# Kernel tuning notes

Hardware: AMD Instinct MI355X
Metric: run time of the kernel (lower is better)

## Reference

```python
import jax, jax.numpy as jnp
import numpy as np

EPS = 1e-5

def _bn(t, gamma, beta):
    # training-mode BatchNorm2d: stats over (B,H,W), biased variance
    mean = jnp.mean(t, axis=(0, 2, 3), keepdims=True)
    var = jnp.var(t, axis=(0, 2, 3), keepdims=True)
    tn = (t - mean) * jax.lax.rsqrt(var + EPS)
    return tn * gamma[None, :, None, None] + beta[None, :, None, None]

def setup_inputs() -> dict:
    key = jax.random.key(0)
    ks = jax.random.split(key, 8)
    B, C, H, W = 16, 256, 64, 64
    u, k, v = 4, 16, 256
    s = 1.0 / np.sqrt(C)
    x = jax.random.normal(ks[0], (B, C, H, W), dtype=jnp.float32)
    Wq = jax.random.normal(ks[1], (k, C), dtype=jnp.float32) * s
    bq = jax.random.normal(ks[2], (k,), dtype=jnp.float32) * 0.01
    Wk = jax.random.normal(ks[3], (u * k, C), dtype=jnp.float32) * s
    bk = jax.random.normal(ks[4], (u * k,), dtype=jnp.float32) * 0.01
    Wv = jax.random.normal(ks[5], (u * v, C), dtype=jnp.float32) * s
    bv = jax.random.normal(ks[6], (u * v,), dtype=jnp.float32) * 0.01
    gamma_q = jnp.ones((k,), dtype=jnp.float32)
    beta_q = jnp.zeros((k,), dtype=jnp.float32)
    gamma_v = jnp.ones((u * v,), dtype=jnp.float32)
    beta_v = jnp.zeros((u * v,), dtype=jnp.float32)
    return {"x": x, "Wq": Wq, "bq": bq, "Wk": Wk, "bk": bk, "Wv": Wv, "bv": bv,
            "gamma_q": gamma_q, "beta_q": beta_q, "gamma_v": gamma_v, "beta_v": beta_v}

def reference(x, Wq, bq, Wk, bk, Wv, bv, gamma_q, beta_q, gamma_v, beta_v):
    B, C, H, W = x.shape
    k = Wq.shape[0]
    u = 4
    v = Wv.shape[0] // u
    # 1x1 convs as channel contractions
    Q = jnp.einsum('oc,bchw->bohw', Wq, x) + bq[None, :, None, None]   # [B,k,H,W]
    K = jnp.einsum('oc,bchw->bohw', Wk, x) + bk[None, :, None, None]   # [B,u*k,H,W]
    V = jnp.einsum('oc,bchw->bohw', Wv, x) + bv[None, :, None, None]   # [B,u*v,H,W]
    Q = _bn(Q, gamma_q, beta_q)
    V = _bn(V, gamma_v, beta_v)
    m = H * W
    Q = Q.reshape(B, k, m)          # [B,k,m]
    K = K.reshape(B, u, k, m)       # [B,u,k,m]
    V = V.reshape(B, u, v, m)       # [B,u,v,m]
    K = jax.nn.softmax(K, axis=3)
    context = jnp.einsum('bukm,buvm->bkv', K, V)   # [B,k,v]
    y = jnp.einsum('bkn,bkv->bvn', Q, context)     # [B,v,m]
    return y.reshape(B, v, H, W)
```

## Files before the change

### kernel.cpp

```cpp
#include <hip/hip_runtime.h>
#include <hip/hip_bf16.h>

typedef short s16x8 __attribute__((ext_vector_type(8)));
typedef short s16x4 __attribute__((ext_vector_type(4)));
typedef float f32x4 __attribute__((ext_vector_type(4)));
typedef unsigned u32;
typedef u32 u32x2 __attribute__((ext_vector_type(2)));

#define DI __device__ __forceinline__

constexpr int BB = 16;
constexpr int CC = 256;
constexpr int MM = 4096;
constexpr int KD = 16;
constexpr int UK = 64;
constexpr float EPSV = 1e-5f;

DI unsigned short f2bf(float f) {
  union { float f; unsigned u; } v; v.f = f;
  unsigned r = v.u + 0x7FFFu + ((v.u >> 16) & 1u);
  return (unsigned short)(r >> 16);
}
DI float bfu(unsigned short u) { union { u32 u; float f; } w; w.u = (u32)u << 16; return w.f; }
DI float bflo(u32 v) { union { u32 u; float f; } w; w.u = v << 16; return w.f; }
DI float bfhi(u32 v) { union { u32 u; float f; } w; w.u = v & 0xFFFF0000u; return w.f; }

__global__ __launch_bounds__(256) void k_cvt(const float* __restrict__ x,
    unsigned short* __restrict__ xbf, float* __restrict__ xsump) {
  int bid = blockIdx.x;
  size_t base = (size_t)bid * MM;
  int t = threadIdx.x;
  float s = 0.f;
#pragma unroll
  for (int i = 0; i < 4; ++i) {
    size_t idx = base + (size_t)(i * 256 + t) * 4;
    float4 v = *(const float4*)(x + idx);
    s16x4 c;
    c[0] = (short)f2bf(v.x); c[1] = (short)f2bf(v.y);
    c[2] = (short)f2bf(v.z); c[3] = (short)f2bf(v.w);
    *(s16x4*)&xbf[idx] = c;
    s += v.x + v.y + v.z + v.w;
  }
#pragma unroll
  for (int o = 32; o; o >>= 1) s += __shfl_down(s, o);
  __shared__ float red[4];
  if ((t & 63) == 0) red[t >> 6] = s;
  __syncthreads();
  if (t == 0) xsump[bid] = red[0] + red[1] + red[2] + red[3];
}

__global__ __launch_bounds__(512) void k_gxx(const unsigned short* __restrict__ xbf,
                                             u32* __restrict__ part) {
  int b = blockIdx.x >> 4, mc = blockIdx.x & 15;
  int m0 = mc * 256;
  __shared__ short lds[2][256 * 72];
  int t = threadIdx.x, w = t >> 6, l = t & 63;
  int wr = w >> 2, wc = w & 3;
  int lrow = l & 15, lk8 = (l >> 4) * 8;
  int srow = t >> 3, sseg = (t & 7) * 8;

  const unsigned short* gsrc = xbf + ((size_t)(b * CC + srow)) * MM + m0 + sseg;

  s16x8 rg[4];
#pragma unroll
  for (int i = 0; i < 4; ++i)
    rg[i] = *(const s16x8*)(gsrc + (size_t)i * 64 * MM);
#pragma unroll
  for (int i = 0; i < 4; ++i)
    *(s16x8*)&lds[0][(srow + i * 64) * 72 + sseg] = rg[i];

  f32x4 acc[8][4];
#pragma unroll
  for (int i = 0; i < 8; ++i)
#pragma unroll
    for (int j = 0; j < 4; ++j) acc[i][j] = (f32x4)0.f;

#pragma unroll
  for (int ks = 0; ks < 4; ++ks) {
    __syncthreads();
    if (ks < 3) {
#pragma unroll
      for (int i = 0; i < 4; ++i)
        rg[i] = *(const s16x8*)(gsrc + (size_t)i * 64 * MM + (ks + 1) * 64);
    }
    int buf = ks & 1;
#pragma unroll
    for (int half = 0; half < 2; ++half) {
      s16x8 af[8], bf[4];
#pragma unroll
      for (int i = 0; i < 8; ++i)
        af[i] = *(const s16x8*)&lds[buf][(wr * 128 + i * 16 + lrow) * 72 + half * 32 + lk8];
#pragma unroll
      for (int j = 0; j < 4; ++j)
        bf[j] = *(const s16x8*)&lds[buf][(wc * 64 + j * 16 + lrow) * 72 + half * 32 + lk8];
#pragma unroll
      for (int i = 0; i < 8; ++i)
#pragma unroll
        for (int j = 0; j < 4; ++j)
          acc[i][j] = __builtin_amdgcn_mfma_f32_16x16x32_bf16(af[i], bf[j], acc[i][j], 0, 0, 0);
    }
    if (ks < 3) {
#pragma unroll
      for (int i = 0; i < 4; ++i)
        *(s16x8*)&lds[buf ^ 1][(srow + i * 64) * 72 + sseg] = rg[i];
    }
  }

  size_t pb = (size_t)blockIdx.x * 32768;
#pragma unroll
  for (int i = 0; i < 8; ++i)
#pragma unroll
    for (int j = 0; j < 4; ++j) {
      int tau = (w * 8 + i) * 4 + j;
      u32x2 pk;
      pk[0] = (u32)f2bf(acc[i][j][0]) | ((u32)f2bf(acc[i][j][1]) << 16);
      pk[1] = (u32)f2bf(acc[i][j][2]) | ((u32)f2bf(acc[i][j][3]) << 16);
      *(u32x2*)&part[pb + tau * 128 + l * 2] = pk;
    }
}

__global__ __launch_bounds__(256) void k_gred(const u32* __restrict__ part,
                                              float* __restrict__ G) {
  int q = blockIdx.x * 256 + threadIdx.x;
  float s0 = 0.f, s1 = 0.f;
#pragma unroll 8
  for (int p = 0; p < 256; ++p) {
    u32 v = part[(size_t)p * 32768 + q];
    s0 += bflo(v);
    s1 += bfhi(v);
  }
  int r2 = q & 1, l = (q >> 1) & 63, tau = q >> 7;
  int j = tau & 3, i = (tau >> 2) & 7, w = tau >> 5;
  int wr = w >> 2, wc = w & 3;
  int row = wr * 128 + i * 16 + (l >> 4) * 4 + r2 * 2;
  int col = wc * 64 + j * 16 + (l & 15);
  G[row * 256 + col] = s0;
  G[(row + 1) * 256 + col] = s1;
}

__global__ __launch_bounds__(256) void k_proj(const unsigned short* __restrict__ xbf,
    const float* __restrict__ Wq, const float* __restrict__ bq,
    const float* __restrict__ Wk, const float* __restrict__ bk,
    unsigned short* __restrict__ Kbf, unsigned short* __restrict__ Qbf,
    float* __restrict__ pstat) {
  int b = blockIdx.x >> 5, mc = blockIdx.x & 31;
  int gm0 = mc * 128;
  __shared__ short wlds[80 * 264];
  __shared__ u32 xt[128 * 17];
  __shared__ float smax[4][64], ssum[4][64];
  int t = threadIdx.x;
  int w = t >> 6, l = t & 63;
  int lrow = l & 15, lk = l >> 4;

#pragma unroll 4
  for (int o = 0; o < 80; ++o) {
    float v = (o < 64) ? Wk[o * CC + t] : Wq[(o - 64) * CC + t];
    wlds[o * 264 + t] = (short)f2bf(v);
  }

  f32x4 acc[5][2];
#pragma unroll
  for (int i = 0; i < 5; ++i) { acc[i][0] = (f32x4)0.f; acc[i][1] = (f32x4)0.f; }

  int c2 = t >> 4;
  int mq = t & 15;

  for (int ks = 0; ks < 8; ++ks) {
    int c0 = ks * 32;
    __syncthreads();
#pragma unroll
    for (int mb = 0; mb < 128; mb += 64) {
      int m = mb + mq * 4;
      const unsigned short* p0 = xbf + ((size_t)(b * CC + c0 + 2 * c2)) * MM + gm0 + m;
      s16x4 v0 = *(const s16x4*)p0;
      s16x4 v1 = *(const s16x4*)(p0 + MM);
      xt[(m + 0) * 17 + c2] = (u32)(unsigned short)v0[0] | ((u32)(unsigned short)v1[0] << 16);
      xt[(m + 1) * 17 + c2] = (u32)(unsigned short)v0[1] | ((u32)(unsigned short)v1[1] << 16);
      xt[(m + 2) * 17 + c2] = (u32)(unsigned short)v0[2] | ((u32)(unsigned short)v1[2] << 16);
      xt[(m + 3) * 17 + c2] = (u32)(unsigned short)v0[3] | ((u32)(unsigned short)v1[3] << 16);
    }
    __syncthreads();
    union { s16x8 v; u32 wd[4]; } bfr[2];
#pragma unroll
    for (int j = 0; j < 2; ++j) {
      int ml = w * 32 + j * 16 + lrow;
#pragma unroll
      for (int i = 0; i < 4; ++i) bfr[j].wd[i] = xt[ml * 17 + lk * 4 + i];
    }
#pragma unroll
    for (int ot = 0; ot < 5; ++ot) {
      s16x8 af = *(const s16x8*)&wlds[(ot * 16 + lrow) * 264 + c0 + lk * 8];
      acc[ot][0] = __builtin_amdgcn_mfma_f32_16x16x32_bf16(af, bfr[0].v, acc[ot][0], 0, 0, 0);
      acc[ot][1] = __builtin_amdgcn_mfma_f32_16x16x32_bf16(af, bfr[1].v, acc[ot][1], 0, 0, 0);
    }
  }

  int mcol = gm0 + w * 32 + lrow;
#pragma unroll
  for (int ot = 0; ot < 4; ++ot)
#pragma unroll
    for (int r = 0; r < 4; ++r) {
      int o = ot * 16 + lk * 4 + r;
      float bias = bk[o];
      unsigned short u0 = f2bf(acc[ot][0][r] + bias);
      unsigned short u1 = f2bf(acc[ot][1][r] + bias);
      size_t rowoff = ((size_t)(b * UK + o)) * MM;
      Kbf[rowoff + mcol] = u0;
      Kbf[rowoff + mcol + 16] = u1;
      float rv0 = bfu(u0), rv1 = bfu(u1);
      float mx = fmaxf(rv0, rv1);
      mx = fmaxf(mx, __shfl_xor(mx, 1));
      mx = fmaxf(mx, __shfl_xor(mx, 2));
      mx = fmaxf(mx, __shfl_xor(mx, 4));
      mx = fmaxf(mx, __shfl_xor(mx, 8));
      float se = __expf(rv0 - mx) + __expf(rv1 - mx);
      se += __shfl_xor(se, 1);
      se += __shfl_xor(se, 2);
      se += __shfl_xor(se, 4);
      se += __shfl_xor(se, 8);
      if (lrow == 0) { smax[w][o] = mx; ssum[w][o] = se; }
    }
#pragma unroll
  for (int r = 0; r < 4; ++r) {
    int oq = lk * 4 + r;
    float bias = bq[oq];
    size_t rowoff = ((size_t)(b * KD + oq)) * MM;
    Qbf[rowoff + mcol] = f2bf(acc[4][0][r] + bias);
    Qbf[rowoff + mcol + 16] = f2bf(acc[4][1][r] + bias);
  }
  __syncthreads();
  if (t < 64) {
    float m0_ = smax[0][t], m1_ = smax[1][t], m2_ = smax[2][t], m3_ = smax[3][t];
    float mm = fmaxf(fmaxf(m0_, m1_), fmaxf(m2_, m3_));
    float ss = ssum[0][t] * __expf(m0_ - mm) + ssum[1][t] * __expf(m1_ - mm) +
               ssum[2][t] * __expf(m2_ - mm) + ssum[3][t] * __expf(m3_ - mm);
    size_t po = ((size_t)blockIdx.x * 64 + t) * 2;
    pstat[po] = mm;
    pstat[po + 1] = ss;
  }
}

__global__ __launch_bounds__(64) void k_pmerge(const float* __restrict__ pstat,
    float* __restrict__ rmax, float* __restrict__ rsum) {
  int b = blockIdx.x, o = threadIdx.x;
  float mm = -3.4e38f;
#pragma unroll 8
  for (int mc = 0; mc < 32; ++mc)
    mm = fmaxf(mm, pstat[((size_t)((b * 32 + mc) * 64 + o)) * 2]);
  float ss = 0.f;
#pragma unroll 8
  for (int mc = 0; mc < 32; ++mc) {
    size_t po = ((size_t)((b * 32 + mc) * 64 + o)) * 2;
    ss += pstat[po + 1] * __expf(pstat[po] - mm);
  }
  rmax[b * 64 + o] = mm;
  rsum[b * 64 + o] = ss;
}

__global__ __launch_bounds__(256) void k_fin(const float* __restrict__ G,
    const float* __restrict__ xsump,
    const float* __restrict__ Wv, const float* __restrict__ bv,
    const float* __restrict__ gv, const float* __restrict__ btv,
    const float* __restrict__ Wq, const float* __restrict__ bq,
    const float* __restrict__ gq, const float* __restrict__ btq,
    float* __restrict__ AV, float* __restrict__ BVa,
    float* __restrict__ AQ, float* __restrict__ BQa) {
  int t = threadIdx.x, w = t >> 6, l = t & 63;
  int o0 = blockIdx.x * 4;
  __shared__ float lw[4][256];
#pragma unroll
  for (int oo = 0; oo < 4; ++oo) {
    int o = o0 + oo;
    lw[oo][t] = (o < 1024) ? Wv[(size_t)o * CC + t] : Wq[(size_t)(o - 1024) * CC + t];
  }
  __syncthreads();

  float4 w4[4];
#pragma unroll
  for (int oo = 0; oo < 4; ++oo) w4[oo] = *(const float4*)&lw[oo][4 * l];

  float qf[4] = {0.f, 0.f, 0.f, 0.f};
#pragma unroll 4
  for (int i = 0; i < 64; ++i) {
    int r = i * 4 + w;
    float4 g4 = *(const float4*)(G + (size_t)r * CC + 4 * l);
#pragma unroll
    for (int oo = 0; oo < 4; ++oo) {
      float d = g4.x * w4[oo].x + g4.y * w4[oo].y + g4.z * w4[oo].z + g4.w * w4[oo].w;
      qf[oo] = fmaf(lw[oo][r], d, qf[oo]);
    }
  }

  float xs = 0.f;
#pragma unroll
  for (int bb = 0; bb < 16; ++bb) xs += xsump[bb * 256 + t];
  float sx[4];
#pragma unroll
  for (int oo = 0; oo < 4; ++oo) sx[oo] = lw[oo][t] * xs;

#pragma unroll
  for (int oo = 0; oo < 4; ++oo)
#pragma unroll
    for (int od = 32; od; od >>= 1) {
      qf[oo] += __shfl_xor(qf[oo], od);
      sx[oo] += __shfl_xor(sx[oo], od);
    }
  __shared__ float rq[4][4], rs[4][4];
  if (l == 0)
#pragma unroll
    for (int oo = 0; oo < 4; ++oo) { rq[w][oo] = qf[oo]; rs[w][oo] = sx[oo]; }
  __syncthreads();
  if (t < 4) {
    int oo = t, o = o0 + oo;
    float q = rq[0][oo] + rq[1][oo] + rq[2][oo] + rq[3][oo];
    float s = rs[0][oo] + rs[1][oo] + rs[2][oo] + rs[3][oo];
    float bias, gamma, beta; float *pa, *pb;
    if (o < 1024) { bias = bv[o]; gamma = gv[o]; beta = btv[o]; pa = AV + o; pb = BVa + o; }
    else { int oi = o - 1024; bias = bq[oi]; gamma = gq[oi]; beta = btq[oi]; pa = AQ + oi; pb = BQa + oi; }
    const float invN = 1.f / 65536.f;
    float mean = s * invN + bias;
    float e2 = q * invN + 2.f * bias * s * invN + bias * bias;
    float var = e2 - mean * mean;
    float a = gamma * rsqrtf(var + EPSV);
    *pa = a;
    *pb = beta - mean * a;
  }
}

__global__ __launch_bounds__(256) void k_xp(const unsigned short* __restrict__ xbf,
    const unsigned short* __restrict__ Kbf, const float* __restrict__ rmax,
    float* __restrict__ xpp) {
  int b = blockIdx.x >> 4, kc = blockIdx.x & 15;
  int kbase = kc * 256;
  __shared__ short la[64][40];
  __shared__ short lb[256][40];
  int t = threadIdx.x, w = t >> 6, l = t & 63;
  int lrow = l & 15, lk = (l >> 4) * 8;

  f32x4 acc[4][4];
#pragma unroll
  for (int i = 0; i < 4; ++i)
#pragma unroll
    for (int j = 0; j < 4; ++j) acc[i][j] = (f32x4)0.f;

  for (int ks = 0; ks < 8; ++ks) {
    int k0 = kbase + ks * 32;
    __syncthreads();
    {
      int r = t >> 2, sg = (t & 3) * 8;
      s16x8 kv = *(const s16x8*)&Kbf[((size_t)(b * UK + r)) * MM + k0 + sg];
      float rm = rmax[b * UK + r];
      s16x8 wv;
#pragma unroll
      for (int i = 0; i < 8; ++i)
        wv[i] = (short)f2bf(__expf(bfu((unsigned short)kv[i]) - rm));
      *(s16x8*)&la[r][sg] = wv;
    }
#pragma unroll
    for (int i = 0; i < 4; ++i) {
      int r = i * 64 + (t >> 2), sg = (t & 3) * 8;
      s16x8 v = *(const s16x8*)&xbf[((size_t)(b * CC + r)) * MM + k0 + sg];
      *(s16x8*)&lb[r][sg] = v;
    }
    __syncthreads();
    s16x8 af[4], bfr[4];
#pragma unroll
    for (int i = 0; i < 4; ++i) af[i] = *(const s16x8*)&la[i * 16 + lrow][lk];
#pragma unroll
    for (int j = 0; j < 4; ++j) bfr[j] = *(const s16x8*)&lb[w * 64 + j * 16 + lrow][lk];
#pragma unroll
    for (int i = 0; i < 4; ++i)
#pragma unroll
      for (int j = 0; j < 4; ++j)
        acc[i][j] = __builtin_amdgcn_mfma_f32_16x16x32_bf16(af[i], bfr[j], acc[i][j], 0, 0, 0);
  }
  float* dst = xpp + (size_t)blockIdx.x * UK * CC;
#pragma unroll
  for (int i = 0; i < 4; ++i)
#pragma unroll
    for (int j = 0; j < 4; ++j)
#pragma unroll
      for (int r = 0; r < 4; ++r) {
        int row = i * 16 + (l >> 4) * 4 + r;
        int col = w * 64 + j * 16 + lrow;
        dst[row * 256 + col] = acc[i][j][r];
      }
}

__global__ __launch_bounds__(256) void k_prep(const float* __restrict__ xpp,
    const float* __restrict__ rsum, const float* __restrict__ Wv,
    const float* __restrict__ AV, unsigned short* __restrict__ xpn,
    unsigned short* __restrict__ wvs) {
  int t = threadIdx.x;
  if (blockIdx.x < 256) {
    int b = blockIdx.x >> 4, kk = blockIdx.x & 15;
    unsigned short* dst = xpn + ((size_t)(b * 16 + kk)) * 1024;
#pragma unroll
    for (int u = 0; u < 4; ++u) {
      int row = u * 16 + kk;
      float s = 0.f;
#pragma unroll
      for (int kc = 0; kc < 16; ++kc)
        s += xpp[((size_t)(b * 16 + kc) * UK + row) * CC + t];
      s /= rsum[b * UK + row];
      dst[u * 256 + t] = f2bf(s);
    }
  } else {
    int ch = blockIdx.x - 256;
    float a = AV[ch];
    wvs[(size_t)ch * CC + t] = f2bf(a * Wv[(size_t)ch * CC + t]);
  }
}

__global__ __launch_bounds__(64) void k_ctx2(const unsigned short* __restrict__ xpn,
    const unsigned short* __restrict__ wvs,
    const float* __restrict__ AV, const float* __restrict__ bv,
    const float* __restrict__ BVa, float* __restrict__ CTX) {
  int mt = blockIdx.x >> 3, nt = blockIdx.x & 7;
  int m0 = mt * 32, n0 = nt * 32;
  int l = threadIdx.x;
  int lrow = l & 15, lk8 = (l >> 4) * 8;

  f32x4 acc[2][2];
#pragma unroll
  for (int i = 0; i < 2; ++i)
#pragma unroll
    for (int j = 0; j < 2; ++j) acc[i][j] = (f32x4)0.f;

#pragma unroll 4
  for (int k0 = 0; k0 < 1024; k0 += 32) {
    int u = k0 >> 8, c0 = k0 & 255;
    s16x8 a0 = *(const s16x8*)&xpn[(size_t)(m0 + lrow) * 1024 + k0 + lk8];
    s16x8 a1 = *(const s16x8*)&xpn[(size_t)(m0 + 16 + lrow) * 1024 + k0 + lk8];
    s16x8 b0 = *(const s16x8*)&wvs[(size_t)(u * 256 + n0 + lrow) * CC + c0 + lk8];
    s16x8 b1 = *(const s16x8*)&wvs[(size_t)(u * 256 + n0 + 16 + lrow) * CC + c0 + lk8];
    acc[0][0] = __builtin_amdgcn_mfma_f32_16x16x32_bf16(a0, b0, acc[0][0], 0, 0, 0);
    acc[0][1] = __builtin_amdgcn_mfma_f32_16x16x32_bf16(a0, b1, acc[0][1], 0, 0, 0);
    acc[1][0] = __builtin_amdgcn_mfma_f32_16x16x32_bf16(a1, b0, acc[1][0], 0, 0, 0);
    acc[1][1] = __builtin_amdgcn_mfma_f32_16x16x32_bf16(a1, b1, acc[1][1], 0, 0, 0);
  }

  float cst[2];
#pragma unroll
  for (int j = 0; j < 2; ++j) {
    int vv = n0 + j * 16 + lrow;
    float s = 0.f;
#pragma unroll
    for (int u = 0; u < 4; ++u) {
      int ch = u * 256 + vv;
      s += AV[ch] * bv[ch] + BVa[ch];
    }
    cst[j] = s;
  }

#pragma unroll
  for (int i = 0; i < 2; ++i)
#pragma unroll
    for (int j = 0; j < 2; ++j)
#pragma unroll
      for (int r = 0; r < 4; ++r) {
        int row = m0 + i * 16 + (l >> 4) * 4 + r;
        int col = n0 + j * 16 + lrow;
        CTX[(size_t)row * 256 + col] = acc[i][j][r] + cst[j];
      }
}

__global__ __launch_bounds__(256) void k_y(const unsigned short* __restrict__ Qbf,
    const float* __restrict__ CTX,
    const float* __restrict__ AQ, const float* __restrict__ BQa,
    float* __restrict__ y) {
  int b = blockIdx.x >> 4, nc = blockIdx.x & 15;
  int m = nc * 256 + threadIdx.x;
  float qn[16];
#pragma unroll
  for (int kk = 0; kk < 16; ++kk)
    qn[kk] = AQ[kk] * bfu(Qbf[((size_t)b * KD + kk) * MM + m]) + BQa[kk];
  const float* cb = CTX + (size_t)b * KD * 256;
  float* yo = y + (size_t)b * 256 * MM + m;
#pragma unroll 4
  for (int vv = 0; vv < 256; ++vv) {
    float acc = 0.f;
#pragma unroll
    for (int kk = 0; kk < 16; ++kk)
      acc = fmaf(qn[kk], cb[kk * 256 + vv], acc);
    yo[(size_t)vv * MM] = acc;
  }
}

extern "C" void kernel_launch(void* const* d_in, const int* in_sizes, int n_in,
                              void* d_out, int out_size, void* d_ws, size_t ws_size,
                              hipStream_t stream) {
  const float* x   = (const float*)d_in[0];
  const float* Wq  = (const float*)d_in[1];
  const float* bq  = (const float*)d_in[2];
  const float* Wk  = (const float*)d_in[3];
  const float* bk  = (const float*)d_in[4];
  const float* Wv  = (const float*)d_in[5];
  const float* bv  = (const float*)d_in[6];
  const float* gq  = (const float*)d_in[7];
  const float* btq = (const float*)d_in[8];
  const float* gv  = (const float*)d_in[9];
  const float* btv = (const float*)d_in[10];
  float* out = (float*)d_out;
  float* ws  = (float*)d_ws;

  float* G     = ws;
  float* XSUMP = ws + 65536;
  float* PSTAT = ws + 69632;
  float* RMAX  = ws + 135168;
  float* RSUM  = ws + 136192;
  float* AV    = ws + 137216;
  float* BVa   = ws + 138240;
  float* AQ    = ws + 139264;
  float* BQa   = ws + 139280;
  float* CTX   = ws + 139520;
  u32*  PART   = (u32*)(ws + 205056);
  float* XPP   = ws + 205056;
  unsigned short* KBf = (unsigned short*)(ws + 4399360);
  unsigned short* QBf = (unsigned short*)(ws + 6496512);
  unsigned short* XBF = (unsigned short*)(ws + 8593664);
  unsigned short* XPN = (unsigned short*)(ws + 16982272);
  unsigned short* WVS = (unsigned short*)(ws + 17113344);

  k_cvt   <<<4096, 256, 0, stream>>>(x, XBF, XSUMP);
  k_gxx   <<<256,  512, 0, stream>>>(XBF, PART);
  k_gred  <<<128,  256, 0, stream>>>(PART, G);
  k_proj  <<<512,  256, 0, stream>>>(XBF, Wq, bq, Wk, bk, KBf, QBf, PSTAT);
  k_pmerge<<<16,   64,  0, stream>>>(PSTAT, RMAX, RSUM);
  k_fin   <<<260,  256, 0, stream>>>(G, XSUMP, Wv, bv, gv, btv, Wq, bq, gq, btq,
                                     AV, BVa, AQ, BQa);
  k_xp    <<<256,  256, 0, stream>>>(XBF, KBf, RMAX, XPP);
  k_prep  <<<1280, 256, 0, stream>>>(XPP, RSUM, Wv, AV, XPN, WVS);
  k_ctx2  <<<64,   64,  0, stream>>>(XPN, WVS, AV, bv, BVa, CTX);
  k_y     <<<256,  256, 0, stream>>>(QBf, CTX, AQ, BQa, out);
}
```

Before: 151.2 us.

## Double-buffer x and weight tiles in k_proj with register prefetch

The projection kernel used to stage all 80x256 weights into LDS before the main loop, then load each x tile with two barriers per k-step. It now streams weight slices per k-step alongside x, using two LDS buffers and register prefetch of the next step's global loads while MFMAs run on the current buffer. This cuts the up-front weight staging, shrinks LDS use and halves the barriers per step. In exchange it uses more registers and converts each weight slice to bf16 again in every block.

```diff
diff --git a/kernel.cpp b/kernel.cpp
--- a/kernel.cpp
+++ b/kernel.cpp
@@ -145,54 +145,111 @@
     float* __restrict__ pstat) {
   int b = blockIdx.x >> 5, mc = blockIdx.x & 31;
   int gm0 = mc * 128;
-  __shared__ short wlds[80 * 264];
-  __shared__ u32 xt[128 * 17];
+  __shared__ u32 xt[2][128 * 17];
+  __shared__ short wb[2][80 * 40];
   __shared__ float smax[4][64], ssum[4][64];
   int t = threadIdx.x;
   int w = t >> 6, l = t & 63;
   int lrow = l & 15, lk = l >> 4;
-
-#pragma unroll 4
-  for (int o = 0; o < 80; ++o) {
-    float v = (o < 64) ? Wk[o * CC + t] : Wq[(o - 64) * CC + t];
-    wlds[o * 264 + t] = (short)f2bf(v);
-  }
-
-  f32x4 acc[5][2];
-#pragma unroll
-  for (int i = 0; i < 5; ++i) { acc[i][0] = (f32x4)0.f; acc[i][1] = (f32x4)0.f; }
-
   int c2 = t >> 4;
   int mq = t & 15;
+  int wrow0 = t >> 3;
+  int wcol = (t & 7) * 4;
+
+  s16x4 xv[2][2];
+  float4 wv[3];
+
+  {
+    const unsigned short* p0 = xbf + ((size_t)(b * CC + 2 * c2)) * MM + gm0 + mq * 4;
+#pragma unroll
+    for (int mb = 0; mb < 2; ++mb) {
+      xv[mb][0] = *(const s16x4*)(p0 + mb * 64);
+      xv[mb][1] = *(const s16x4*)(p0 + mb * 64 + MM);
+    }
+#pragma unroll
+    for (int rep = 0; rep < 3; ++rep) {
+      int row = rep * 32 + wrow0;
+      if (row < 80)
+        wv[rep] = *(const float4*)((row < 64 ? Wk + (size_t)row * CC
+                                             : Wq + (size_t)(row - 64) * CC) + wcol);
+    }
+#pragma unroll
+    for (int mb = 0; mb < 2; ++mb) {
+      int m = mb * 64 + mq * 4;
+#pragma unroll
+      for (int i = 0; i < 4; ++i)
+        xt[0][(m + i) * 17 + c2] =
+            (u32)(unsigned short)xv[mb][0][i] | ((u32)(unsigned short)xv[mb][1][i] << 16);
+    }
+#pragma unroll
+    for (int rep = 0; rep < 3; ++rep) {
+      int row = rep * 32 + wrow0;
+      if (row < 80) {
+        s16x4 wc4;
+        wc4[0] = (short)f2bf(wv[rep].x); wc4[1] = (short)f2bf(wv[rep].y);
+        wc4[2] = (short)f2bf(wv[rep].z); wc4[3] = (short)f2bf(wv[rep].w);
+        *(s16x4*)&wb[0][row * 40 + wcol] = wc4;
+      }
+    }
+  }
+  __syncthreads();
+
+  f32x4 acc[5][2];
+#pragma unroll
+  for (int i = 0; i < 5; ++i) { acc[i][0] = (f32x4)0.f; acc[i][1] = (f32x4)0.f; }
 
   for (int ks = 0; ks < 8; ++ks) {
-    int c0 = ks * 32;
-    __syncthreads();
-#pragma unroll
-    for (int mb = 0; mb < 128; mb += 64) {
-      int m = mb + mq * 4;
-      const unsigned short* p0 = xbf + ((size_t)(b * CC + c0 + 2 * c2)) * MM + gm0 + m;
-      s16x4 v0 = *(const s16x4*)p0;
-      s16x4 v1 = *(const s16x4*)(p0 + MM);
-      xt[(m + 0) * 17 + c2] = (u32)(unsigned short)v0[0] | ((u32)(unsigned short)v1[0] << 16);
-      xt[(m + 1) * 17 + c2] = (u32)(unsigned short)v0[1] | ((u32)(unsigned short)v1[1] << 16);
-      xt[(m + 2) * 17 + c2] = (u32)(unsigned short)v0[2] | ((u32)(unsigned short)v1[2] << 16);
-      xt[(m + 3) * 17 + c2] = (u32)(unsigned short)v0[3] | ((u32)(unsigned short)v1[3] << 16);
-    }
-    __syncthreads();
+    int buf = ks & 1;
+    if (ks < 7) {
+      int c0 = (ks + 1) * 32;
+      const unsigned short* p0 = xbf + ((size_t)(b * CC + c0 + 2 * c2)) * MM + gm0 + mq * 4;
+#pragma unroll
+      for (int mb = 0; mb < 2; ++mb) {
+        xv[mb][0] = *(const s16x4*)(p0 + mb * 64);
+        xv[mb][1] = *(const s16x4*)(p0 + mb * 64 + MM);
+      }
+#pragma unroll
+      for (int rep = 0; rep < 3; ++rep) {
+        int row = rep * 32 + wrow0;
+        if (row < 80)
+          wv[rep] = *(const float4*)((row < 64 ? Wk + (size_t)row * CC
+                                               : Wq + (size_t)(row - 64) * CC) + c0 + wcol);
+      }
+    }
     union { s16x8 v; u32 wd[4]; } bfr[2];
 #pragma unroll
     for (int j = 0; j < 2; ++j) {
       int ml = w * 32 + j * 16 + lrow;
 #pragma unroll
-      for (int i = 0; i < 4; ++i) bfr[j].wd[i] = xt[ml * 17 + lk * 4 + i];
+      for (int i = 0; i < 4; ++i) bfr[j].wd[i] = xt[buf][ml * 17 + lk * 4 + i];
     }
 #pragma unroll
     for (int ot = 0; ot < 5; ++ot) {
-      s16x8 af = *(const s16x8*)&wlds[(ot * 16 + lrow) * 264 + c0 + lk * 8];
+      s16x8 af = *(const s16x8*)&wb[buf][(ot * 16 + lrow) * 40 + lk * 8];
       acc[ot][0] = __builtin_amdgcn_mfma_f32_16x16x32_bf16(af, bfr[0].v, acc[ot][0], 0, 0, 0);
       acc[ot][1] = __builtin_amdgcn_mfma_f32_16x16x32_bf16(af, bfr[1].v, acc[ot][1], 0, 0, 0);
     }
+    if (ks < 7) {
+#pragma unroll
+      for (int mb = 0; mb < 2; ++mb) {
+        int m = mb * 64 + mq * 4;
+#pragma unroll
+        for (int i = 0; i < 4; ++i)
+          xt[buf ^ 1][(m + i) * 17 + c2] =
+              (u32)(unsigned short)xv[mb][0][i] | ((u32)(unsigned short)xv[mb][1][i] << 16);
+      }
+#pragma unroll
+      for (int rep = 0; rep < 3; ++rep) {
+        int row = rep * 32 + wrow0;
+        if (row < 80) {
+          s16x4 wc4;
+          wc4[0] = (short)f2bf(wv[rep].x); wc4[1] = (short)f2bf(wv[rep].y);
+          wc4[2] = (short)f2bf(wv[rep].z); wc4[3] = (short)f2bf(wv[rep].w);
+          *(s16x4*)&wb[buf ^ 1][row * 40 + wcol] = wc4;
+        }
+      }
+    }
+    __syncthreads();
   }
 
   int mcol = gm0 + w * 32 + lrow;
```

Result: faster. 145.5 us (-3.8%).
